# Kernel tuning notes

Measured on AMD Instinct MI355X. Metric: run time of the kernel, lower is better.

The kernel has to match this reference:

```python
import jax, jax.numpy as jnp
import numpy as np

N, D, F, E, K = 16384, 512, 2048, 8, 2


def setup_inputs() -> dict:
    key = jax.random.key(0)
    ks = jax.random.split(key, 5)
    s = 0.02
    return {
        "x": jax.random.normal(ks[0], (N, D), dtype=jnp.float32),
        "gate_w": jax.random.normal(ks[1], (D, E), dtype=jnp.float32) * s,
        "w1": jax.random.normal(ks[2], (E, D, F), dtype=jnp.float32) * s,
        "w2": jax.random.normal(ks[3], (E, F, D), dtype=jnp.float32) * s,
        "w3": jax.random.normal(ks[4], (E, D, F), dtype=jnp.float32) * s,
    }


def reference(x, gate_w, w1, w2, w3):
    # gate: [N, E] logits -> top-k experts per token
    logits = x @ gate_w
    top_vals, top_idx = jax.lax.top_k(logits, K)          # [N, K]
    # softmax over the selected-k logits in float32 (matches F.softmax dtype=float)
    weights = jax.nn.softmax(top_vals.astype(jnp.float32), axis=-1).astype(x.dtype)
    out = jnp.zeros_like(x)
    for e in range(E):
        # combine weight for expert e per token (0 if not selected)
        m = jnp.sum(jnp.where(top_idx == e, weights, 0.0), axis=-1)  # [N]
        h = jax.nn.silu(x @ w1[e]) * (x @ w3[e])                     # [N, F]
        out = out + m[:, None] * (h @ w2[e])
    return out
```

## Files before the change

### kernel.cpp

```cpp
#include <hip/hip_runtime.h>
#include <hip/hip_bf16.h>
#include <math.h>

#define N_TOK 16384
#define DIM   512
#define FDIM  2048
#define NEXP  8
#define TOPK  2
#define PAIRS (N_TOK*TOPK)
#define MAX_TILES (PAIRS/128 + NEXP)

typedef __hip_bfloat16 bf16;
typedef __attribute__((ext_vector_type(8))) short bf16x8;
typedef __attribute__((ext_vector_type(4))) float f32x4;
typedef __attribute__((ext_vector_type(8))) short s16x8;

__device__ __forceinline__ short f2bf(float f){
  union { float f; unsigned u; } v; v.f = f;
  unsigned r = v.u + 0x7fffu + ((v.u >> 16) & 1u);
  return (short)(r >> 16);
}
__device__ __forceinline__ float bf2f(short s){
  union { unsigned u; float f; } v; v.u = ((unsigned)(unsigned short)s) << 16;
  return v.f;
}
__device__ __forceinline__ void g2l16(const void* g, void* l){
  __builtin_amdgcn_global_load_lds(
      (const __attribute__((address_space(1))) unsigned int*)g,
      (__attribute__((address_space(3))) unsigned int*)l, 16, 0, 0);
}

__global__ __launch_bounds__(512) void k_gate(const float* __restrict__ x,
    const float* __restrict__ gw, int* __restrict__ tidx, float* __restrict__ tw){
  __shared__ float gwT[NEXP][DIM];
  int tid = threadIdx.x;
  #pragma unroll
  for(int i=0;i<8;i++){
    int idx = tid + 512*i;
    gwT[idx&7][idx>>3] = gw[idx];
  }
  __syncthreads();
  int lane = tid & 63, wid = tid >> 6;
  int t = blockIdx.x*8 + wid;
  const float* xr = x + (size_t)t*DIM;
  float acc[NEXP];
  #pragma unroll
  for(int e=0;e<NEXP;e++) acc[e]=0.f;
  #pragma unroll
  for(int c=0;c<8;c++){
    float xv = xr[c*64 + lane];
    #pragma unroll
    for(int e=0;e<NEXP;e++) acc[e] += xv * gwT[e][c*64+lane];
  }
  #pragma unroll
  for(int off=32; off; off>>=1){
    #pragma unroll
    for(int e=0;e<NEXP;e++) acc[e] += __shfl_xor(acc[e], off);
  }
  if(lane==0){
    int e0=0; float v0=acc[0];
    #pragma unroll
    for(int e=1;e<NEXP;e++) if(acc[e]>v0){v0=acc[e]; e0=e;}
    int e1=-1; float v1=-1e30f;
    #pragma unroll
    for(int e=0;e<NEXP;e++) if(e!=e0 && acc[e]>v1){v1=acc[e]; e1=e;}
    float z = expf(v1-v0);
    float w0 = 1.f/(1.f+z);
    tidx[t*2]=e0; tidx[t*2+1]=e1;
    tw[t*2]=w0; tw[t*2+1]=1.f-w0;
  }
}

__global__ __launch_bounds__(256) void k_count(const int* __restrict__ tidx,
                                               int* __restrict__ counts){
  __shared__ int h[NEXP];
  if(threadIdx.x<NEXP) h[threadIdx.x]=0;
  __syncthreads();
  int i0 = blockIdx.x*1024 + threadIdx.x;
  #pragma unroll
  for(int k=0;k<4;k++) atomicAdd(&h[tidx[i0 + 256*k]], 1);
  __syncthreads();
  if(threadIdx.x<NEXP) atomicAdd(&counts[threadIdx.x], h[threadIdx.x]);
}

__global__ void k_route(const int* __restrict__ counts, int* __restrict__ offsets,
    int* __restrict__ ntiles, int* __restrict__ te, int* __restrict__ tb,
    int* __restrict__ ts){
  if(threadIdx.x==0){
    int off=0, nt=0;
    for(int e=0;e<NEXP;e++){
      offsets[e]=off;
      int c=counts[e];
      int tiles=(c+127)>>7;
      for(int i=0;i<tiles;i++){ te[nt]=e; tb[nt]=off+(i<<7); ts[nt]=off+c; nt++; }
      off += c;
    }
    *ntiles=nt;
  }
}

__global__ __launch_bounds__(256) void k_scatter(const int* __restrict__ tidx,
    const int* __restrict__ offsets, int* __restrict__ fill,
    int* __restrict__ token_list, int* __restrict__ posmap){
  __shared__ int lcnt[NEXP], lbase[NEXP];
  if(threadIdx.x<NEXP) lcnt[threadIdx.x]=0;
  __syncthreads();
  int i = blockIdx.x*256 + threadIdx.x;
  int e = tidx[i];
  int rank = atomicAdd(&lcnt[e], 1);
  __syncthreads();
  if(threadIdx.x<NEXP) lbase[threadIdx.x] = atomicAdd(&fill[threadIdx.x], lcnt[threadIdx.x]);
  __syncthreads();
  int pos = offsets[e] + lbase[e] + rank;
  token_list[pos] = i>>1;
  posmap[i] = pos;
}

__global__ __launch_bounds__(256) void k_cast(const float* __restrict__ x,
                                              bf16* __restrict__ xb){
  int i = blockIdx.x*256 + threadIdx.x;
  const float* p = x + (size_t)i*8;
  f32x4 a = *(const f32x4*)p;
  f32x4 b = *(const f32x4*)(p+4);
  s16x8 r;
  r[0]=f2bf(a[0]); r[1]=f2bf(a[1]); r[2]=f2bf(a[2]); r[3]=f2bf(a[3]);
  r[4]=f2bf(b[0]); r[5]=f2bf(b[1]); r[6]=f2bf(b[2]); r[7]=f2bf(b[3]);
  *(s16x8*)((short*)xb + (size_t)i*8) = r;
}

__global__ __launch_bounds__(256) void k_transpose(const float* __restrict__ src,
    bf16* __restrict__ dst, int R, int C){
  __shared__ float tile[32][33];
  const float* s = src + (size_t)blockIdx.z*R*C;
  short* d = (short*)dst + (size_t)blockIdx.z*R*C;
  int c0 = blockIdx.x*32, r0 = blockIdx.y*32;
  int tx = threadIdx.x & 31, ty = threadIdx.x >> 5;
  #pragma unroll
  for(int i=0;i<4;i++) tile[ty+8*i][tx] = s[(size_t)(r0+ty+8*i)*C + c0+tx];
  __syncthreads();
  #pragma unroll
  for(int i=0;i<4;i++) d[(size_t)(c0+ty+8*i)*R + r0+tx] = f2bf(tile[tx][ty+8*i]);
}

__global__ __launch_bounds__(256,3) void k_gemmA(const bf16* __restrict__ xb,
    const bf16* __restrict__ w1T, const bf16* __restrict__ w3T,
    const int* __restrict__ ntiles, const int* __restrict__ te,
    const int* __restrict__ tb, const int* __restrict__ ts,
    const int* __restrict__ token_list, bf16* __restrict__ H){
  int tile = blockIdx.x;
  if(tile >= *ntiles) return;
  int e = te[tile], base = tb[tile], send = ts[tile];
  int f0 = blockIdx.y*64;
  __shared__ short As[2*128*32];
  __shared__ short B1s[2*64*32];
  __shared__ short B3s[2*64*32];
  int tid = threadIdx.x;
  int srow0 = tid>>2, srow1 = 64 + (tid>>2);
  int sx = (tid>>3)&3;
  int scol = ((tid&3) ^ sx)*8;
  int r0g = base + srow0, r1g = base + srow1;
  int tok0 = token_list[(r0g < send) ? r0g : base];
  int tok1 = token_list[(r1g < send) ? r1g : base];
  const short* gA0 = (const short*)xb + (size_t)tok0*DIM + scol;
  const short* gA1 = (const short*)xb + (size_t)tok1*DIM + scol;
  const short* gB1 = (const short*)w1T + ((size_t)e*FDIM + f0 + srow0)*DIM + scol;
  const short* gB3 = (const short*)w3T + ((size_t)e*FDIM + f0 + srow0)*DIM + scol;
  char* dA  = (char*)As  + tid*16;
  char* dB1 = (char*)B1s + tid*16;
  char* dB3 = (char*)B3s + tid*16;
  int wid = tid>>6, lane = tid&63;
  int wr = wid>>1, wc = wid&1;
  int lrow = lane&15, g = lane>>4;
  f32x4 acc1[4][2] = {};
  f32x4 acc3[4][2] = {};
  g2l16(gA0, dA);
  g2l16(gA1, dA + 4096);
  g2l16(gB1, dB1);
  g2l16(gB3, dB3);
  __syncthreads();
  int p = 0;
  for(int t=0; t<16; t++){
    if(t<15){
      int d1 = (t+1)*32;
      int ao = (p^1)*8192, bo = (p^1)*4096;
      g2l16(gA0 + d1, dA + ao);
      g2l16(gA1 + d1, dA + ao + 4096);
      g2l16(gB1 + d1, dB1 + bo);
      g2l16(gB3 + d1, dB3 + bo);
    }
    const short* Ab  = As  + p*4096;
    const short* B1b = B1s + p*2048;
    const short* B3b = B3s + p*2048;
    bf16x8 af[4], b1f[2], b3f[2];
    #pragma unroll
    for(int m=0;m<4;m++){
      int r = wr*64 + m*16 + lrow;
      af[m] = *(const bf16x8*)&Ab[r*32 + ((g ^ ((r>>1)&3))<<3)];
    }
    #pragma unroll
    for(int n=0;n<2;n++){
      int r = wc*32 + n*16 + lrow;
      int c = (g ^ ((r>>1)&3))<<3;
      b1f[n] = *(const bf16x8*)&B1b[r*32 + c];
      b3f[n] = *(const bf16x8*)&B3b[r*32 + c];
    }
    #pragma unroll
    for(int m=0;m<4;m++){
      #pragma unroll
      for(int n=0;n<2;n++){
        acc1[m][n] = __builtin_amdgcn_mfma_f32_16x16x32_bf16(af[m], b1f[n], acc1[m][n], 0,0,0);
        acc3[m][n] = __builtin_amdgcn_mfma_f32_16x16x32_bf16(af[m], b3f[n], acc3[m][n], 0,0,0);
      }
    }
    __syncthreads();
    p ^= 1;
  }
  #pragma unroll
  for(int m=0;m<4;m++){
    int r0 = base + wr*64 + m*16 + ((lane>>4)<<2);
    #pragma unroll
    for(int n=0;n<2;n++){
      int col = f0 + wc*32 + n*16 + lrow;
      #pragma unroll
      for(int j=0;j<4;j++){
        if(r0+j < send){
          float a = acc1[m][n][j];
          float h = a * (1.f/(1.f+__expf(-a))) * acc3[m][n][j];
          ((short*)H)[(size_t)(r0+j)*FDIM + col] = f2bf(h);
        }
      }
    }
  }
}

__global__ __launch_bounds__(256,3) void k_gemmB(const bf16* __restrict__ H,
    const bf16* __restrict__ w2T, const int* __restrict__ ntiles,
    const int* __restrict__ te, const int* __restrict__ tb,
    const int* __restrict__ ts, bf16* __restrict__ O){
  int tile = blockIdx.x;
  if(tile >= *ntiles) return;
  int e = te[tile], base = tb[tile], send = ts[tile];
  int n0 = blockIdx.y*128;
  __shared__ short As[2*128*32];
  __shared__ short Bs[2*128*32];
  int tid = threadIdx.x;
  int srow0 = tid>>2, srow1 = 64 + (tid>>2);
  int sx = (tid>>3)&3;
  int scol = ((tid&3) ^ sx)*8;
  int r0g = base + srow0, r1g = base + srow1;
  int ar0 = (r0g < send) ? r0g : base;
  int ar1 = (r1g < send) ? r1g : base;
  const short* gA0 = (const short*)H + (size_t)ar0*FDIM + scol;
  const short* gA1 = (const short*)H + (size_t)ar1*FDIM + scol;
  const short* gB0 = (const short*)w2T + ((size_t)e*DIM + n0 + srow0)*FDIM + scol;
  const short* gB1 = (const short*)w2T + ((size_t)e*DIM + n0 + srow1)*FDIM + scol;
  char* dA = (char*)As + tid*16;
  char* dB = (char*)Bs + tid*16;
  int wid = tid>>6, lane = tid&63, wr = wid>>1, wc = wid&1;
  int lrow = lane&15, g = lane>>4;
  f32x4 acc[4][4] = {};
  g2l16(gA0, dA);
  g2l16(gA1, dA + 4096);
  g2l16(gB0, dB);
  g2l16(gB1, dB + 4096);
  __syncthreads();
  int p = 0;
  for(int t=0; t<64; t++){
    if(t<63){
      int d1 = (t+1)*32;
      int o = (p^1)*8192;
      g2l16(gA0 + d1, dA + o);
      g2l16(gA1 + d1, dA + o + 4096);
      g2l16(gB0 + d1, dB + o);
      g2l16(gB1 + d1, dB + o + 4096);
    }
    const short* Ab = As + p*4096;
    const short* Bb = Bs + p*4096;
    bf16x8 af[4], bfr[4];
    #pragma unroll
    for(int m=0;m<4;m++){
      int r = wr*64 + m*16 + lrow;
      af[m] = *(const bf16x8*)&Ab[r*32 + ((g ^ ((r>>1)&3))<<3)];
    }
    #pragma unroll
    for(int n=0;n<4;n++){
      int r = wc*64 + n*16 + lrow;
      bfr[n] = *(const bf16x8*)&Bb[r*32 + ((g ^ ((r>>1)&3))<<3)];
    }
    #pragma unroll
    for(int m=0;m<4;m++){
      #pragma unroll
      for(int n=0;n<4;n++)
        acc[m][n] = __builtin_amdgcn_mfma_f32_16x16x32_bf16(af[m], bfr[n], acc[m][n], 0,0,0);
    }
    __syncthreads();
    p ^= 1;
  }
  #pragma unroll
  for(int m=0;m<4;m++){
    #pragma unroll
    for(int j=0;j<4;j++){
      int r2 = base + wr*64 + m*16 + ((lane>>4)<<2) + j;
      if(r2 < send){
        #pragma unroll
        for(int n=0;n<4;n++){
          int col = n0 + wc*64 + n*16 + lrow;
          ((short*)O)[(size_t)r2*DIM + col] = f2bf(acc[m][n][j]);
        }
      }
    }
  }
}

__global__ __launch_bounds__(256) void k_combine(const bf16* __restrict__ O,
    const int* __restrict__ posmap, const float* __restrict__ tw,
    float* __restrict__ out){
  int lane = threadIdx.x & 63, wid = threadIdx.x >> 6;
  int t = blockIdx.x*4 + wid;
  int p0 = posmap[2*t], p1 = posmap[2*t+1];
  float w0 = tw[2*t], w1 = tw[2*t+1];
  s16x8 a = *(const s16x8*)((const short*)O + (size_t)p0*DIM + lane*8);
  s16x8 b = *(const s16x8*)((const short*)O + (size_t)p1*DIM + lane*8);
  f32x4 r0, r1;
  #pragma unroll
  for(int j=0;j<4;j++) r0[j] = w0*bf2f(a[j]) + w1*bf2f(b[j]);
  #pragma unroll
  for(int j=0;j<4;j++) r1[j] = w0*bf2f(a[4+j]) + w1*bf2f(b[4+j]);
  float* o = out + (size_t)t*DIM + lane*8;
  *(f32x4*)o = r0;
  *(f32x4*)(o+4) = r1;
}

extern "C" void kernel_launch(void* const* d_in, const int* in_sizes, int n_in,
                              void* d_out, int out_size, void* d_ws, size_t ws_size,
                              hipStream_t stream){
  const float* x  = (const float*)d_in[0];
  const float* gw = (const float*)d_in[1];
  const float* w1 = (const float*)d_in[2];
  const float* w2 = (const float*)d_in[3];
  const float* w3 = (const float*)d_in[4];
  float* out = (float*)d_out;
  char* ws = (char*)d_ws;

  int* cw = (int*)ws;
  int* counts = cw;
  int* fill   = cw + 8;
  int* offsets= cw + 16;
  int* ntiles = cw + 24;
  int* te = cw + 32;
  int* tb = cw + 296;
  int* ts = cw + 560;
  int* tidx       = cw + 824;
  int* token_list = cw + 824 + PAIRS;
  int* posmap     = cw + 824 + 2*PAIRS;
  float* tw       = (float*)(cw + 824 + 3*PAIRS);

  const size_t MB = 1u<<20;
  bf16* xb  = (bf16*)(ws + 1*MB);
  bf16* w1T = (bf16*)(ws + 17*MB);
  bf16* w3T = (bf16*)(ws + 33*MB);
  bf16* w2T = (bf16*)(ws + 49*MB);
  bf16* Hbuf= (bf16*)(ws + 65*MB);
  bf16* Obuf= (bf16*)(ws + 17*MB);
  size_t needed = 65*MB + (size_t)PAIRS*FDIM*2u;
  if(ws_size < needed) return;

  hipMemsetAsync(d_ws, 0, 64, stream);

  k_gate<<<N_TOK/8, 512, 0, stream>>>(x, gw, tidx, tw);
  k_count<<<PAIRS/1024, 256, 0, stream>>>(tidx, counts);
  k_route<<<1, 64, 0, stream>>>(counts, offsets, ntiles, te, tb, ts);
  k_scatter<<<PAIRS/256, 256, 0, stream>>>(tidx, offsets, fill, token_list, posmap);
  k_cast<<<(N_TOK*DIM/8)/256, 256, 0, stream>>>(x, xb);
  k_transpose<<<dim3(FDIM/32, DIM/32, NEXP), 256, 0, stream>>>(w1, w1T, DIM, FDIM);
  k_transpose<<<dim3(FDIM/32, DIM/32, NEXP), 256, 0, stream>>>(w3, w3T, DIM, FDIM);
  k_transpose<<<dim3(DIM/32, FDIM/32, NEXP), 256, 0, stream>>>(w2, w2T, FDIM, DIM);
  k_gemmA<<<dim3(MAX_TILES, FDIM/64), 256, 0, stream>>>(xb, w1T, w3T, ntiles, te, tb, ts, token_list, Hbuf);
  k_gemmB<<<dim3(MAX_TILES, DIM/128), 256, 0, stream>>>(Hbuf, w2T, ntiles, te, tb, ts, Obuf);
  k_combine<<<N_TOK/4, 256, 0, stream>>>(Obuf, posmap, tw, out);
}
```

Baseline: 511.6 us.

## Deepen LDS prefetch with explicit waitcnt pipelining and remap tile order in grouped GEMMs

Restructures both expert GEMM main loops so global-to-LDS loads run two K-steps ahead. Fragments are read into registers first, then the freed buffer is refilled while MFMAs run, with explicit vmcnt/lgkmcnt waits and raw barriers in place of __syncthreads. It also remaps blockIdx.x to tile through an interleave (bx&7)*33+(bx>>3) to spread experts across the launch order. The hand-written waitcnts add fragility, and the hard-coded 33 assumes a particular grid size.

```diff
diff --git a/kernel.cpp b/kernel.cpp
--- a/kernel.cpp
+++ b/kernel.cpp
@@ -14,6 +14,12 @@
 typedef __attribute__((ext_vector_type(8))) short bf16x8;
 typedef __attribute__((ext_vector_type(4))) float f32x4;
 typedef __attribute__((ext_vector_type(8))) short s16x8;
+
+#define WAIT_VM4   asm volatile("s_waitcnt vmcnt(4)" ::: "memory")
+#define WAIT_VM0   asm volatile("s_waitcnt vmcnt(0)" ::: "memory")
+#define WAIT_LGKM0 asm volatile("s_waitcnt lgkmcnt(0)" ::: "memory")
+#define SFENCE     __builtin_amdgcn_sched_barrier(0)
+#define BAR        __builtin_amdgcn_s_barrier()
 
 __device__ __forceinline__ short f2bf(float f){
   union { float f; unsigned u; } v; v.f = f;
@@ -142,12 +148,23 @@
   for(int i=0;i<4;i++) d[(size_t)(c0+ty+8*i)*R + r0+tx] = f2bf(tile[tx][ty+8*i]);
 }
 
+#define GA_STAGE(t, pb) do{ int _d=(t)*32; int _ao=(pb)*8192, _bo=(pb)*4096; \
+  g2l16(gA0+_d, dA+_ao); g2l16(gA1+_d, dA+_ao+4096); \
+  g2l16(gB1+_d, dB1+_bo); g2l16(gB3+_d, dB3+_bo); }while(0)
+#define GA_READ(pb) do{ const short* Ab=As+(pb)*4096; const short* B1b=B1s+(pb)*2048; const short* B3b=B3s+(pb)*2048; \
+  _Pragma("unroll") for(int m=0;m<4;m++){ int r=wr*64+m*16+lrow; af[m]=*(const bf16x8*)&Ab[r*32+((g^((r>>1)&3))<<3)]; } \
+  _Pragma("unroll") for(int n=0;n<2;n++){ int r=wc*32+n*16+lrow; int c=(g^((r>>1)&3))<<3; \
+    b1f[n]=*(const bf16x8*)&B1b[r*32+c]; b3f[n]=*(const bf16x8*)&B3b[r*32+c]; } }while(0)
+#define GA_MMA() do{ _Pragma("unroll") for(int m=0;m<4;m++){ _Pragma("unroll") for(int n=0;n<2;n++){ \
+  acc1[m][n]=__builtin_amdgcn_mfma_f32_16x16x32_bf16(af[m],b1f[n],acc1[m][n],0,0,0); \
+  acc3[m][n]=__builtin_amdgcn_mfma_f32_16x16x32_bf16(af[m],b3f[n],acc3[m][n],0,0,0);}} }while(0)
 __global__ __launch_bounds__(256,3) void k_gemmA(const bf16* __restrict__ xb,
     const bf16* __restrict__ w1T, const bf16* __restrict__ w3T,
     const int* __restrict__ ntiles, const int* __restrict__ te,
     const int* __restrict__ tb, const int* __restrict__ ts,
     const int* __restrict__ token_list, bf16* __restrict__ H){
-  int tile = blockIdx.x;
+  int bx = blockIdx.x;
+  int tile = (bx&7)*33 + (bx>>3);
   if(tile >= *ntiles) return;
   int e = te[tile], base = tb[tile], send = ts[tile];
   int f0 = blockIdx.y*64;
@@ -173,47 +190,34 @@
   int lrow = lane&15, g = lane>>4;
   f32x4 acc1[4][2] = {};
   f32x4 acc3[4][2] = {};
-  g2l16(gA0, dA);
-  g2l16(gA1, dA + 4096);
-  g2l16(gB1, dB1);
-  g2l16(gB3, dB3);
-  __syncthreads();
+  GA_STAGE(0,0);
+  GA_STAGE(1,1);
+  WAIT_VM4; SFENCE; BAR;
   int p = 0;
-  for(int t=0; t<16; t++){
-    if(t<15){
-      int d1 = (t+1)*32;
-      int ao = (p^1)*8192, bo = (p^1)*4096;
-      g2l16(gA0 + d1, dA + ao);
-      g2l16(gA1 + d1, dA + ao + 4096);
-      g2l16(gB1 + d1, dB1 + bo);
-      g2l16(gB3 + d1, dB3 + bo);
-    }
-    const short* Ab  = As  + p*4096;
-    const short* B1b = B1s + p*2048;
-    const short* B3b = B3s + p*2048;
+  #pragma unroll 1
+  for(int t=0; t<14; ++t){
     bf16x8 af[4], b1f[2], b3f[2];
-    #pragma unroll
-    for(int m=0;m<4;m++){
-      int r = wr*64 + m*16 + lrow;
-      af[m] = *(const bf16x8*)&Ab[r*32 + ((g ^ ((r>>1)&3))<<3)];
-    }
-    #pragma unroll
-    for(int n=0;n<2;n++){
-      int r = wc*32 + n*16 + lrow;
-      int c = (g ^ ((r>>1)&3))<<3;
-      b1f[n] = *(const bf16x8*)&B1b[r*32 + c];
-      b3f[n] = *(const bf16x8*)&B3b[r*32 + c];
-    }
-    #pragma unroll
-    for(int m=0;m<4;m++){
-      #pragma unroll
-      for(int n=0;n<2;n++){
-        acc1[m][n] = __builtin_amdgcn_mfma_f32_16x16x32_bf16(af[m], b1f[n], acc1[m][n], 0,0,0);
-        acc3[m][n] = __builtin_amdgcn_mfma_f32_16x16x32_bf16(af[m], b3f[n], acc3[m][n], 0,0,0);
-      }
-    }
-    __syncthreads();
+    GA_READ(p);
+    WAIT_LGKM0; SFENCE;
+    BAR;
+    GA_STAGE(t+2, p);
+    GA_MMA();
+    WAIT_VM4; SFENCE;
+    BAR;
     p ^= 1;
+  }
+  {
+    bf16x8 af[4], b1f[2], b3f[2];
+    GA_READ(p);
+    GA_MMA();
+    WAIT_VM0; SFENCE;
+    BAR;
+    p ^= 1;
+  }
+  {
+    bf16x8 af[4], b1f[2], b3f[2];
+    GA_READ(p);
+    GA_MMA();
   }
   #pragma unroll
   for(int m=0;m<4;m++){
@@ -233,11 +237,20 @@
   }
 }
 
+#define GB_STAGE(t, pb) do{ int _d=(t)*32; int _o=(pb)*8192; \
+  g2l16(gA0+_d, dA+_o); g2l16(gA1+_d, dA+_o+4096); \
+  g2l16(gB0+_d, dB+_o); g2l16(gB1+_d, dB+_o+4096); }while(0)
+#define GB_READ(pb) do{ const short* Ab=As+(pb)*4096; const short* Bb=Bs+(pb)*4096; \
+  _Pragma("unroll") for(int m=0;m<4;m++){ int r=wr*64+m*16+lrow; af[m]=*(const bf16x8*)&Ab[r*32+((g^((r>>1)&3))<<3)]; } \
+  _Pragma("unroll") for(int n=0;n<4;n++){ int r=wc*64+n*16+lrow; bfr[n]=*(const bf16x8*)&Bb[r*32+((g^((r>>1)&3))<<3)]; } }while(0)
+#define GB_MMA() do{ _Pragma("unroll") for(int m=0;m<4;m++){ _Pragma("unroll") for(int n=0;n<4;n++) \
+  acc[m][n]=__builtin_amdgcn_mfma_f32_16x16x32_bf16(af[m],bfr[n],acc[m][n],0,0,0); } }while(0)
 __global__ __launch_bounds__(256,3) void k_gemmB(const bf16* __restrict__ H,
     const bf16* __restrict__ w2T, const int* __restrict__ ntiles,
     const int* __restrict__ te, const int* __restrict__ tb,
     const int* __restrict__ ts, bf16* __restrict__ O){
-  int tile = blockIdx.x;
+  int bx = blockIdx.x;
+  int tile = (bx&7)*33 + (bx>>3);
   if(tile >= *ntiles) return;
   int e = te[tile], base = tb[tile], send = ts[tile];
   int n0 = blockIdx.y*128;
@@ -259,42 +272,34 @@
   int wid = tid>>6, lane = tid&63, wr = wid>>1, wc = wid&1;
   int lrow = lane&15, g = lane>>4;
   f32x4 acc[4][4] = {};
-  g2l16(gA0, dA);
-  g2l16(gA1, dA + 4096);
-  g2l16(gB0, dB);
-  g2l16(gB1, dB + 4096);
-  __syncthreads();
+  GB_STAGE(0,0);
+  GB_STAGE(1,1);
+  WAIT_VM4; SFENCE; BAR;
   int p = 0;
-  for(int t=0; t<64; t++){
-    if(t<63){
-      int d1 = (t+1)*32;
-      int o = (p^1)*8192;
-      g2l16(gA0 + d1, dA + o);
-      g2l16(gA1 + d1, dA + o + 4096);
-      g2l16(gB0 + d1, dB + o);
-      g2l16(gB1 + d1, dB + o + 4096);
-    }
-    const short* Ab = As + p*4096;
-    const short* Bb = Bs + p*4096;
+  #pragma unroll 1
+  for(int t=0; t<62; ++t){
     bf16x8 af[4], bfr[4];
-    #pragma unroll
-    for(int m=0;m<4;m++){
-      int r = wr*64 + m*16 + lrow;
-      af[m] = *(const bf16x8*)&Ab[r*32 + ((g ^ ((r>>1)&3))<<3)];
-    }
-    #pragma unroll
-    for(int n=0;n<4;n++){
-      int r = wc*64 + n*16 + lrow;
-      bfr[n] = *(const bf16x8*)&Bb[r*32 + ((g ^ ((r>>1)&3))<<3)];
-    }
-    #pragma unroll
-    for(int m=0;m<4;m++){
-      #pragma unroll
-      for(int n=0;n<4;n++)
-        acc[m][n] = __builtin_amdgcn_mfma_f32_16x16x32_bf16(af[m], bfr[n], acc[m][n], 0,0,0);
-    }
-    __syncthreads();
+    GB_READ(p);
+    WAIT_LGKM0; SFENCE;
+    BAR;
+    GB_STAGE(t+2, p);
+    GB_MMA();
+    WAIT_VM4; SFENCE;
+    BAR;
     p ^= 1;
+  }
+  {
+    bf16x8 af[4], bfr[4];
+    GB_READ(p);
+    GB_MMA();
+    WAIT_VM0; SFENCE;
+    BAR;
+    p ^= 1;
+  }
+  {
+    bf16x8 af[4], bfr[4];
+    GB_READ(p);
+    GB_MMA();
   }
   #pragma unroll
   for(int m=0;m<4;m++){
```

Result: no change. 502.6 us (-1.8%).
